# Optimization experiments

Measured on AMD Instinct MI355X. Metric: run time of the kernel, lower is better.

Reference implementation:

```python
import jax, jax.numpy as jnp
import numpy as np

B, H, N, DH = 4096, 4, 1024, 256  # batch, heads, codes per head, per-head dim
DECAY, EPS, COMMIT = 0.99, 1e-5, 0.25


def setup_inputs() -> dict:
    key = jax.random.key(0)
    k1, k2, k3, k4 = jax.random.split(key, 4)
    return {
        "inputs": jax.random.normal(k1, (B, 1, H * DH), dtype=jnp.float32),
        "emb_w": jax.random.normal(k2, (H, N, DH), dtype=jnp.float32),
        "ema_w": jax.random.normal(k3, (H, N, DH), dtype=jnp.float32),
        "cluster_size": jnp.zeros((H, N), dtype=jnp.float32),
        "trans_w": jax.random.normal(k4, (H, N, N), dtype=jnp.float32) * 0.03,
    }


def reference(inputs, emb_w, ema_w, cluster_size, trans_w):
    sg = jax.lax.stop_gradient
    x = inputs[:, 0, :].reshape(B, H, DH)  # split heads
    quant, codes = [], []
    prev_probs = None
    for h in range(H):
        xi = x[:, h]                       # [B, DH]
        w = emb_w[h]                       # [N, DH]
        # squared euclidean distances [B, N]
        d = (jnp.sum(xi * xi, axis=1, keepdims=True)
             + jnp.sum(w * w, axis=1)
             - 2.0 * xi @ w.T)
        logits = -sg(d)
        if prev_probs is not None:  # transition prior from previous head (detached)
            logits = logits + sg(prev_probs @ trans_w[h].T)
        probs = jax.nn.softmax(logits, axis=-1)
        prev_probs = probs
        # EMA codebook update (training mode)
        cs = cluster_size[h] * DECAY + (1.0 - DECAY) * jnp.sum(probs, axis=0)
        n = jnp.sum(cs)
        cs = (cs + EPS) / (n + N * EPS) * n
        dw = probs.T @ xi                  # [N, DH]
        ew = ema_w[h] * DECAY + (1.0 - DECAY) * dw
        new_w = ew / cs[:, None]           # updated codebook used for quantization
        codes.append(jnp.argmax(probs, axis=-1))
        quant.append(probs @ sg(new_w))    # soft-EM quantization, detached codebook
    quantized = jnp.stack(quant, axis=1).reshape(inputs.shape)  # [B,1,H*DH]
    q_loss = jnp.mean((quantized - sg(inputs)) ** 2, axis=(-1, -2))
    e_loss = jnp.mean((sg(quantized) - inputs) ** 2, axis=(-1, -2))
    loss = COMMIT * e_loss + q_loss        # [B]
    quantized = inputs + sg(quantized - inputs)  # straight-through
    vq_codes = jnp.stack(codes, axis=1)    # [B, H]
    return loss, quantized, vq_codes
```

## Files before the change

### kernel.cpp

```cpp
#include <hip/hip_runtime.h>
#include <hip/hip_bf16.h>
#include <math.h>

#define BB 4096
#define HH 4
#define NN 1024
#define DHD 256
#define XLD 1024
#define DECAY 0.99f
#define OMD 0.01f
#define EPSV 1e-5f

typedef __attribute__((ext_vector_type(8))) short bf16x8;
typedef __attribute__((ext_vector_type(4))) float f32x4;
typedef unsigned short u16;

#define MFMA(a, b, c) __builtin_amdgcn_mfma_f32_16x16x32_bf16((a), (b), (c), 0, 0, 0)


static __device__ __forceinline__ u16 f2bf(float x) {
    union { __hip_bfloat16 b; u16 u; } c; c.b = __float2bfloat16(x); return c.u;
}
static __device__ __forceinline__ float bf2f(u16 u) {
    union { __hip_bfloat16 b; u16 u; } c; c.u = u; return __bfloat162float(c.b);
}
static __device__ __forceinline__ void split3(float x, u16& h, u16& m, u16& l) {
    h = f2bf(x);
    float r = x - bf2f(h);
    m = f2bf(r);
    float r2 = r - bf2f(m);
    l = f2bf(r2);
}

__global__ __launch_bounds__(256) void k_prep_x(const float* __restrict__ in,
        u16* __restrict__ xph, u16* __restrict__ xpm, u16* __restrict__ xpl,
        u16* __restrict__ xtph, u16* __restrict__ xtpl) {
    __shared__ float T[64][68];
    const int t = threadIdx.x, lane = t & 63, wid = t >> 6;
    const int q = lane >> 4, mr = lane & 15;
    const int c0 = blockIdx.x * 64, i0 = blockIdx.y * 64;
    const int h = c0 >> 8, kl0 = c0 & 255;
#pragma unroll
    for (int rep = 0; rep < 4; rep++) {
        int id = t + 256 * rep;
        int row = id >> 4, c4 = (id & 15) * 4;
        float4 v = *(const float4*)(in + (size_t)(i0 + row) * XLD + c0 + c4);
        *(float4*)&T[row][c4] = v;
    }
    __syncthreads();
    for (int f = wid; f < 8; f += 4) {
        int a = f >> 1, b = f & 1;
        bf16x8 vh, vm, vl;
#pragma unroll
        for (int e = 0; e < 8; e++) {
            float x2 = 2.f * T[16 * a + mr][b * 32 + q * 8 + e];
            u16 hh, mm, ll; split3(x2, hh, mm, ll);
            vh[e] = (short)hh; vm[e] = (short)mm; vl[e] = (short)ll;
        }
        size_t o = (size_t)h * BB * DHD +
                   ((size_t)((i0 >> 4) + a) * 8 + ((kl0 >> 5) + b)) * 512 + lane * 8;
        *(bf16x8*)(xph + o) = vh;
        *(bf16x8*)(xpm + o) = vm;
        *(bf16x8*)(xpl + o) = vl;
    }
    for (int f = wid; f < 8; f += 4) {
        int a = f >> 1, b = f & 1;
        bf16x8 vh, vl;
#pragma unroll
        for (int e = 0; e < 8; e++) {
            float x = T[b * 32 + q * 8 + e][16 * a + mr];
            u16 hh = f2bf(x);
            u16 ll = f2bf(x - bf2f(hh));
            vh[e] = (short)hh; vl[e] = (short)ll;
        }
        size_t o = (size_t)h * DHD * BB +
                   ((size_t)((kl0 >> 4) + a) * 128 + ((i0 >> 5) + b)) * 512 + lane * 8;
        *(bf16x8*)(xtph + o) = vh;
        *(bf16x8*)(xtpl + o) = vl;
    }
}

__global__ __launch_bounds__(256) void k_prep_w(const float* __restrict__ w,
        u16* __restrict__ wph, u16* __restrict__ wpm, u16* __restrict__ wpl) {
    const int t = threadIdx.x, lane = t & 63, wid = t >> 6;
    const int q = lane >> 4, mr = lane & 15;
    int fid = blockIdx.x * 4 + wid;
    int kt = fid & 7, jt = (fid >> 3) & 63, h = fid >> 9;
    const float* src = w + (size_t)(h * NN + jt * 16 + mr) * DHD + kt * 32 + q * 8;
    bf16x8 vh, vm, vl;
#pragma unroll
    for (int e = 0; e < 8; e++) {
        u16 hh, mm, ll; split3(src[e], hh, mm, ll);
        vh[e] = (short)hh; vm[e] = (short)mm; vl[e] = (short)ll;
    }
    size_t o = (size_t)h * NN * DHD + ((size_t)jt * 8 + kt) * 512 + lane * 8;
    *(bf16x8*)(wph + o) = vh;
    *(bf16x8*)(wpm + o) = vm;
    *(bf16x8*)(wpl + o) = vl;
}

__global__ __launch_bounds__(256) void k_prep_t(const float* __restrict__ w,
        u16* __restrict__ tph, u16* __restrict__ tpl) {
    const int t = threadIdx.x, lane = t & 63, wid = t >> 6;
    const int q = lane >> 4, mr = lane & 15;
    int fid = blockIdx.x * 4 + wid;
    int kt = fid & 31, jt = (fid >> 5) & 63, h = fid >> 11;
    const float* src = w + (size_t)(h * NN + jt * 16 + mr) * NN + kt * 32 + q * 8;
    bf16x8 vh, vl;
#pragma unroll
    for (int e = 0; e < 8; e++) {
        u16 hh = f2bf(src[e]);
        u16 ll = f2bf(src[e] - bf2f(hh));
        vh[e] = (short)hh; vl[e] = (short)ll;
    }
    size_t o = (size_t)h * NN * NN + ((size_t)jt * 32 + kt) * 512 + lane * 8;
    *(bf16x8*)(tph + o) = vh;
    *(bf16x8*)(tpl + o) = vl;
}

__global__ __launch_bounds__(256) void k_wsq(const float* __restrict__ emb,
                                             float* __restrict__ wsq) {
    int wave = threadIdx.x >> 6;
    int lane = threadIdx.x & 63;
    int row  = blockIdx.x * 4 + wave;
    const float* w = emb + (size_t)row * DHD;
    float4 v = *(const float4*)(w + lane * 4);
    float s = v.x * v.x + v.y * v.y + v.z * v.z + v.w * v.w;
    for (int off = 32; off; off >>= 1) s += __shfl_down(s, off);
    if (lane == 0) wsq[row] = s;
}

template <int HASPREV>
__global__ __launch_bounds__(256) void k_logits_frag(
        const u16* __restrict__ Xph, const u16* __restrict__ Xpm, const u16* __restrict__ Xpl,
        const u16* __restrict__ Wph, const u16* __restrict__ Wpm, const u16* __restrict__ Wpl,
        const float* __restrict__ wsq,
        const u16* __restrict__ Pph, const u16* __restrict__ Ppl,
        const u16* __restrict__ Tph, const u16* __restrict__ Tpl,
        float* __restrict__ L) {
    const int t = threadIdx.x;
    const int lane = t & 63, wid = t >> 6;
    const int wmi = wid >> 1, wn = wid & 1;
    const int q = lane >> 4, mr = lane & 15;
    const int j0 = blockIdx.x * 64, i0 = blockIdx.y * 64;
    const int it0 = (i0 >> 4) + wmi * 2;
    const int jt0 = (j0 >> 4) + wn * 2;
    const int lo = lane * 8;

    f32x4 zero = {0.f, 0.f, 0.f, 0.f};
    f32x4 s[2][2], acc2[2][2];
#pragma unroll
    for (int mt = 0; mt < 2; mt++)
#pragma unroll
        for (int nt = 0; nt < 2; nt++) { s[mt][nt] = zero; acc2[mt][nt] = zero; }

    {
        const u16 *ahp[2], *amp[2], *alp[2], *bhp[2], *bmp[2], *blp[2];
#pragma unroll
        for (int mt = 0; mt < 2; mt++) {
            size_t b = (size_t)(it0 + mt) * 8 * 512 + lo;
            ahp[mt] = Xph + b; amp[mt] = Xpm + b; alp[mt] = Xpl + b;
        }
#pragma unroll
        for (int nt = 0; nt < 2; nt++) {
            size_t b = (size_t)(jt0 + nt) * 8 * 512 + lo;
            bhp[nt] = Wph + b; bmp[nt] = Wpm + b; blp[nt] = Wpl + b;
        }
#pragma unroll 2
        for (int kt = 0; kt < 8; kt++) {
            bf16x8 ah[2], am[2], al[2], bh[2], bm[2], bl[2];
#pragma unroll
            for (int mt = 0; mt < 2; mt++) {
                ah[mt] = *(const bf16x8*)(ahp[mt] + kt * 512);
                am[mt] = *(const bf16x8*)(amp[mt] + kt * 512);
                al[mt] = *(const bf16x8*)(alp[mt] + kt * 512);
            }
#pragma unroll
            for (int nt = 0; nt < 2; nt++) {
                bh[nt] = *(const bf16x8*)(bhp[nt] + kt * 512);
                bm[nt] = *(const bf16x8*)(bmp[nt] + kt * 512);
                bl[nt] = *(const bf16x8*)(blp[nt] + kt * 512);
            }
#pragma unroll
            for (int mt = 0; mt < 2; mt++)
#pragma unroll
                for (int nt = 0; nt < 2; nt++) {
                    f32x4 fresh = MFMA(ah[mt], bh[nt], zero);
                    s[mt][nt] += fresh;
                    acc2[mt][nt] = MFMA(ah[mt], bm[nt], acc2[mt][nt]);
                    acc2[mt][nt] = MFMA(am[mt], bh[nt], acc2[mt][nt]);
                    acc2[mt][nt] = MFMA(ah[mt], bl[nt], acc2[mt][nt]);
                    acc2[mt][nt] = MFMA(am[mt], bm[nt], acc2[mt][nt]);
                    acc2[mt][nt] = MFMA(al[mt], bh[nt], acc2[mt][nt]);
                }
        }
    }

    if (HASPREV) {
        const u16 *ahp[2], *alp[2], *bhp[2], *blp[2];
#pragma unroll
        for (int mt = 0; mt < 2; mt++) {
            size_t b = (size_t)(it0 + mt) * 32 * 512 + lo;
            ahp[mt] = Pph + b; alp[mt] = Ppl + b;
        }
#pragma unroll
        for (int nt = 0; nt < 2; nt++) {
            size_t b = (size_t)(jt0 + nt) * 32 * 512 + lo;
            bhp[nt] = Tph + b; blp[nt] = Tpl + b;
        }
#pragma unroll 2
        for (int kt = 0; kt < 32; kt++) {
            bf16x8 ah[2], al[2], bh[2], bl[2];
#pragma unroll
            for (int mt = 0; mt < 2; mt++) {
                ah[mt] = *(const bf16x8*)(ahp[mt] + kt * 512);
                al[mt] = *(const bf16x8*)(alp[mt] + kt * 512);
            }
#pragma unroll
            for (int nt = 0; nt < 2; nt++) {
                bh[nt] = *(const bf16x8*)(bhp[nt] + kt * 512);
                bl[nt] = *(const bf16x8*)(blp[nt] + kt * 512);
            }
#pragma unroll
            for (int mt = 0; mt < 2; mt++)
#pragma unroll
                for (int nt = 0; nt < 2; nt++) {
                    acc2[mt][nt] = MFMA(ah[mt], bh[nt], acc2[mt][nt]);
                    acc2[mt][nt] = MFMA(ah[mt], bl[nt], acc2[mt][nt]);
                    acc2[mt][nt] = MFMA(al[mt], bh[nt], acc2[mt][nt]);
                }
        }
    }

    float wq[2];
#pragma unroll
    for (int nt = 0; nt < 2; nt++) wq[nt] = wsq[j0 + wn * 32 + nt * 16 + mr];
#pragma unroll
    for (int mt = 0; mt < 2; mt++)
#pragma unroll
        for (int nt = 0; nt < 2; nt++)
#pragma unroll
            for (int r = 0; r < 4; r++) {
                int gi = i0 + wmi * 32 + mt * 16 + q * 4 + r;
                int gj = j0 + wn * 32 + nt * 16 + mr;
                L[(size_t)gi * NN + gj] = (s[mt][nt][r] + acc2[mt][nt][r]) - wq[nt];
            }
}

__global__ __launch_bounds__(256) void k_softmax(const float* __restrict__ L,
                                                 u16* __restrict__ Ph,
                                                 u16* __restrict__ Pl,
                                                 float* __restrict__ codes,
                                                 int h) {
    __shared__ float smax[256];
    __shared__ int   sidx[256];
    const int i = blockIdx.x;
    const int t = threadIdx.x;
    const float* row = L + (size_t)i * NN;

    float v[4];
    float m = -INFINITY;
    int   mi = 0;
#pragma unroll
    for (int q4 = 0; q4 < 4; q4++) {
        int j = q4 * 256 + t;
        v[q4] = row[j];
        if (v[q4] > m) { m = v[q4]; mi = j; }
    }
    smax[t] = m; sidx[t] = mi;
    __syncthreads();
    for (int s = 128; s; s >>= 1) {
        if (t < s) {
            float o = smax[t + s]; int oi = sidx[t + s];
            if (o > smax[t] || (o == smax[t] && oi < sidx[t])) { smax[t] = o; sidx[t] = oi; }
        }
        __syncthreads();
    }
    m = smax[0];
    int code = sidx[0];
    __syncthreads();

    float s = 0.f;
#pragma unroll
    for (int q4 = 0; q4 < 4; q4++) { v[q4] = expf(v[q4] - m); s += v[q4]; }
    smax[t] = s;
    __syncthreads();
    for (int ss = 128; ss; ss >>= 1) {
        if (t < ss) smax[t] += smax[t + ss];
        __syncthreads();
    }
    float inv = 1.0f / smax[0];
#pragma unroll
    for (int q4 = 0; q4 < 4; q4++) {
        float pv = v[q4] * inv;
        u16 hb = f2bf(pv);
        Ph[(size_t)i * NN + q4 * 256 + t] = hb;
        Pl[(size_t)i * NN + q4 * 256 + t] = f2bf(pv - bf2f(hb));
    }
    if (t == 0) codes[(size_t)i * HH + h] = (float)code;
}

__global__ __launch_bounds__(256) void k_packP(const u16* __restrict__ Ph,
        const u16* __restrict__ Pl, u16* __restrict__ Pph, u16* __restrict__ Ppl) {
    const int t = threadIdx.x, lane = t & 63, wid = t >> 6;
    const int q = lane >> 4, mr = lane & 15;
    int fid = blockIdx.x * 4 + wid;
    int kt = fid & 31, it = fid >> 5;
    size_t si = (size_t)(it * 16 + mr) * NN + kt * 32 + q * 8;
    bf16x8 vh = *(const bf16x8*)(Ph + si);
    bf16x8 vl = *(const bf16x8*)(Pl + si);
    size_t o = ((size_t)it * 32 + kt) * 512 + lane * 8;
    *(bf16x8*)(Pph + o) = vh;
    *(bf16x8*)(Ppl + o) = vl;
}

__global__ __launch_bounds__(256) void k_packPT(const u16* __restrict__ Ph,
        const u16* __restrict__ Pl, u16* __restrict__ PTph, u16* __restrict__ PTpl) {
    __shared__ u16 U[64][72];
    const int t = threadIdx.x, lane = t & 63, wid = t >> 6;
    const int q = lane >> 4, mr = lane & 15;
    const int j0 = blockIdx.x * 64, i0 = blockIdx.y * 64;
    for (int pass = 0; pass < 2; pass++) {
        const u16* src = pass ? Pl : Ph;
        u16* dst = pass ? PTpl : PTph;
        if (pass) __syncthreads();
#pragma unroll
        for (int rep = 0; rep < 2; rep++) {
            int id = t + 256 * rep;
            int row = id >> 3, c8 = (id & 7) * 8;
            *(bf16x8*)&U[row][c8] = *(const bf16x8*)(src + (size_t)(i0 + row) * NN + j0 + c8);
        }
        __syncthreads();
        for (int f = wid; f < 8; f += 4) {
            int a = f >> 1, b = f & 1;
            bf16x8 v;
#pragma unroll
            for (int e = 0; e < 8; e++) v[e] = (short)U[b * 32 + q * 8 + e][16 * a + mr];
            size_t o = ((size_t)((j0 >> 4) + a) * 128 + ((i0 >> 5) + b)) * 512 + lane * 8;
            *(bf16x8*)(dst + o) = v;
        }
    }
}

__global__ __launch_bounds__(256) void k_colsum(const u16* __restrict__ Ph,
                                                const u16* __restrict__ Pl,
                                                float* __restrict__ colsum) {
    int j  = blockIdx.x * 256 + threadIdx.x;
    int i0 = blockIdx.y * 256;
    float s = 0.f;
    for (int i = i0; i < i0 + 256; i++)
        s += bf2f(Ph[(size_t)i * NN + j]) + bf2f(Pl[(size_t)i * NN + j]);
    atomicAdd(&colsum[j], s);
}

__global__ __launch_bounds__(1024) void k_cs(const float* __restrict__ cluster_size,
                                             const float* __restrict__ colsum,
                                             float* __restrict__ csn, int h) {
    __shared__ float red[1024];
    int j = threadIdx.x;
    float cs = cluster_size[h * NN + j] * DECAY + OMD * colsum[j];
    red[j] = cs;
    __syncthreads();
    for (int s = 512; s; s >>= 1) {
        if (j < s) red[j] += red[j + s];
        __syncthreads();
    }
    float n = red[0];
    csn[j] = (cs + EPSV) / (n + NN * EPSV) * n;
}

__global__ __launch_bounds__(256) void k_dw_frag(
        const u16* __restrict__ PTph, const u16* __restrict__ PTpl,
        const u16* __restrict__ XTph, const u16* __restrict__ XTpl,
        float* __restrict__ partial) {
    const int t = threadIdx.x;
    const int lane = t & 63, wid = t >> 6;
    const int wmi = wid >> 1, wn = wid & 1;
    const int q = lane >> 4, mr = lane & 15;
    const int kd0 = blockIdx.x * 64, j0 = blockIdx.y * 64;
    const int z = blockIdx.z;
    const int jt0 = (j0 >> 4) + wmi * 2;
    const int kdt0 = (kd0 >> 4) + wn * 2;
    const int lo = lane * 8;

    f32x4 zero = {0.f, 0.f, 0.f, 0.f};
    f32x4 acc[2][2];
#pragma unroll
    for (int mt = 0; mt < 2; mt++)
#pragma unroll
        for (int nt = 0; nt < 2; nt++) acc[mt][nt] = zero;

    const u16 *ahp[2], *alp[2], *bhp[2], *blp[2];
#pragma unroll
    for (int mt = 0; mt < 2; mt++) {
        size_t b = ((size_t)(jt0 + mt) * 128 + z * 8) * 512 + lo;
        ahp[mt] = PTph + b; alp[mt] = PTpl + b;
    }
#pragma unroll
    for (int nt = 0; nt < 2; nt++) {
        size_t b = ((size_t)(kdt0 + nt) * 128 + z * 8) * 512 + lo;
        bhp[nt] = XTph + b; blp[nt] = XTpl + b;
    }
#pragma unroll 2
    for (int kt = 0; kt < 8; kt++) {
        bf16x8 ah[2], al[2], bh[2], bl[2];
#pragma unroll
        for (int mt = 0; mt < 2; mt++) {
            ah[mt] = *(const bf16x8*)(ahp[mt] + kt * 512);
            al[mt] = *(const bf16x8*)(alp[mt] + kt * 512);
        }
#pragma unroll
        for (int nt = 0; nt < 2; nt++) {
            bh[nt] = *(const bf16x8*)(bhp[nt] + kt * 512);
            bl[nt] = *(const bf16x8*)(blp[nt] + kt * 512);
        }
#pragma unroll
        for (int mt = 0; mt < 2; mt++)
#pragma unroll
            for (int nt = 0; nt < 2; nt++) {
                acc[mt][nt] = MFMA(ah[mt], bh[nt], acc[mt][nt]);
                acc[mt][nt] = MFMA(ah[mt], bl[nt], acc[mt][nt]);
                acc[mt][nt] = MFMA(al[mt], bh[nt], acc[mt][nt]);
            }
    }
#pragma unroll
    for (int mt = 0; mt < 2; mt++)
#pragma unroll
        for (int nt = 0; nt < 2; nt++)
#pragma unroll
            for (int r = 0; r < 4; r++) {
                int gj = j0 + wmi * 32 + mt * 16 + q * 4 + r;
                int gk = kd0 + wn * 32 + nt * 16 + mr;
                atomicAdd(&partial[(size_t)gj * DHD + gk], acc[mt][nt][r]);
            }
}

__global__ __launch_bounds__(256) void k_neww_ep(const float* __restrict__ partial,
        const float* __restrict__ ema, const float* __restrict__ csn,
        u16* __restrict__ NWph, u16* __restrict__ NWpl) {
    __shared__ float T[64][68];
    const int t = threadIdx.x, lane = t & 63, wid = t >> 6;
    const int q = lane >> 4, mr = lane & 15;
    const int j0 = blockIdx.x * 64, kd0 = blockIdx.y * 64;
#pragma unroll
    for (int rep = 0; rep < 4; rep++) {
        int id = t + 256 * rep;
        int jr = id >> 4, c4 = (id & 15) * 4;
        float4 pp = *(const float4*)(partial + (size_t)(j0 + jr) * DHD + kd0 + c4);
        float4 ee = *(const float4*)(ema + (size_t)(j0 + jr) * DHD + kd0 + c4);
        float ic = 1.0f / csn[j0 + jr];
        float4 v;
        v.x = (ee.x * DECAY + OMD * pp.x) * ic;
        v.y = (ee.y * DECAY + OMD * pp.y) * ic;
        v.z = (ee.z * DECAY + OMD * pp.z) * ic;
        v.w = (ee.w * DECAY + OMD * pp.w) * ic;
        *(float4*)&T[jr][c4] = v;
    }
    __syncthreads();
    for (int f = wid; f < 8; f += 4) {
        int a = f >> 1, b = f & 1;
        bf16x8 vh, vl;
#pragma unroll
        for (int e = 0; e < 8; e++) {
            float x = T[b * 32 + q * 8 + e][16 * a + mr];
            u16 hh = f2bf(x);
            u16 ll = f2bf(x - bf2f(hh));
            vh[e] = (short)hh; vl[e] = (short)ll;
        }
        size_t o = ((size_t)((kd0 >> 4) + a) * 32 + ((j0 >> 5) + b)) * 512 + lane * 8;
        *(bf16x8*)(NWph + o) = vh;
        *(bf16x8*)(NWpl + o) = vl;
    }
}

__global__ __launch_bounds__(256) void k_quant_frag(
        const u16* __restrict__ Pph, const u16* __restrict__ Ppl,
        const u16* __restrict__ NWph, const u16* __restrict__ NWpl,
        float* __restrict__ outq, int h) {
    const int t = threadIdx.x;
    const int lane = t & 63, wid = t >> 6;
    const int wmi = wid >> 1, wn = wid & 1;
    const int q = lane >> 4, mr = lane & 15;
    const int kd0 = blockIdx.x * 64, i0 = blockIdx.y * 64;
    const int z = blockIdx.z;
    const int it0 = (i0 >> 4) + wmi * 2;
    const int kdt0 = (kd0 >> 4) + wn * 2;
    const int lo = lane * 8;

    f32x4 zero = {0.f, 0.f, 0.f, 0.f};
    f32x4 acc[2][2];
#pragma unroll
    for (int mt = 0; mt < 2; mt++)
#pragma unroll
        for (int nt = 0; nt < 2; nt++) acc[mt][nt] = zero;

    const u16 *ahp[2], *alp[2], *bhp[2], *blp[2];
#pragma unroll
    for (int mt = 0; mt < 2; mt++) {
        size_t b = ((size_t)(it0 + mt) * 32 + z * 8) * 512 + lo;
        ahp[mt] = Pph + b; alp[mt] = Ppl + b;
    }
#pragma unroll
    for (int nt = 0; nt < 2; nt++) {
        size_t b = ((size_t)(kdt0 + nt) * 32 + z * 8) * 512 + lo;
        bhp[nt] = NWph + b; blp[nt] = NWpl + b;
    }
#pragma unroll 2
    for (int kt = 0; kt < 8; kt++) {
        bf16x8 ah[2], al[2], bh[2], bl[2];
#pragma unroll
        for (int mt = 0; mt < 2; mt++) {
            ah[mt] = *(const bf16x8*)(ahp[mt] + kt * 512);
            al[mt] = *(const bf16x8*)(alp[mt] + kt * 512);
        }
#pragma unroll
        for (int nt = 0; nt < 2; nt++) {
            bh[nt] = *(const bf16x8*)(bhp[nt] + kt * 512);
            bl[nt] = *(const bf16x8*)(blp[nt] + kt * 512);
        }
#pragma unroll
        for (int mt = 0; mt < 2; mt++)
#pragma unroll
            for (int nt = 0; nt < 2; nt++) {
                acc[mt][nt] = MFMA(ah[mt], bh[nt], acc[mt][nt]);
                acc[mt][nt] = MFMA(ah[mt], bl[nt], acc[mt][nt]);
                acc[mt][nt] = MFMA(al[mt], bh[nt], acc[mt][nt]);
            }
    }
#pragma unroll
    for (int mt = 0; mt < 2; mt++)
#pragma unroll
        for (int nt = 0; nt < 2; nt++)
#pragma unroll
            for (int r = 0; r < 4; r++) {
                int gi = i0 + wmi * 32 + mt * 16 + q * 4 + r;
                int gk = kd0 + wn * 32 + nt * 16 + mr;
                atomicAdd(&outq[(size_t)gi * XLD + h * DHD + gk], acc[mt][nt][r]);
            }
}

__global__ __launch_bounds__(256) void k_loss(const float* __restrict__ x,
                                              const float* __restrict__ qv,
                                              float* __restrict__ loss) {
    __shared__ float red[256];
    const int i = blockIdx.x, t = threadIdx.x;
    const float* xr = x + (size_t)i * XLD;
    const float* qr = qv + (size_t)i * XLD;
    float s = 0.f;
#pragma unroll
    for (int q4 = 0; q4 < 4; q4++) {
        int k = q4 * 256 + t;
        float d = qr[k] - xr[k];
        s += d * d;
    }
    red[t] = s;
    __syncthreads();
    for (int ss = 128; ss; ss >>= 1) {
        if (t < ss) red[t] += red[t + ss];
        __syncthreads();
    }
    if (t == 0) loss[i] = 1.25f * red[0] * (1.0f / 1024.0f);
}

extern "C" void kernel_launch(void* const* d_in, const int* in_sizes, int n_in,
                              void* d_out, int out_size, void* d_ws, size_t ws_size,
                              hipStream_t stream) {
    const float* inputs = (const float*)d_in[0];
    const float* emb    = (const float*)d_in[1];
    const float* ema    = (const float*)d_in[2];
    const float* csz    = (const float*)d_in[3];
    const float* trans  = (const float*)d_in[4];

    float* out   = (float*)d_out;
    float* loss  = out;
    float* quant = out + BB;
    float* codes = out + BB + (size_t)BB * XLD;

    char* p = (char*)d_ws;
    float* L = (float*)p; p += (size_t)BB * NN * 4;
    u16* PTph = (u16*)L;
    u16* PTpl = PTph + (size_t)BB * NN;
    u16* Ph   = (u16*)p; p += (size_t)BB * NN * 2;
    u16* Pl   = (u16*)p; p += (size_t)BB * NN * 2;
    u16* Pph  = (u16*)p; p += (size_t)BB * NN * 2;
    u16* Ppl  = (u16*)p; p += (size_t)BB * NN * 2;
    u16* Xph  = (u16*)p; p += (size_t)BB * XLD * 2;
    u16* Xpm  = (u16*)p; p += (size_t)BB * XLD * 2;
    u16* Xpl  = (u16*)p; p += (size_t)BB * XLD * 2;
    u16* XTph = (u16*)p; p += (size_t)XLD * BB * 2;
    u16* XTpl = (u16*)p; p += (size_t)XLD * BB * 2;
    u16* Wph  = (u16*)p; p += (size_t)HH * NN * DHD * 2;
    u16* Wpm  = (u16*)p; p += (size_t)HH * NN * DHD * 2;
    u16* Wpl  = (u16*)p; p += (size_t)HH * NN * DHD * 2;
    u16* Tph  = (u16*)p; p += (size_t)HH * NN * NN * 2;
    u16* Tpl  = (u16*)p; p += (size_t)HH * NN * NN * 2;
    u16* NWph = (u16*)p; p += (size_t)DHD * NN * 2;
    u16* NWpl = (u16*)p; p += (size_t)DHD * NN * 2;
    float* wsq    = (float*)p; p += (size_t)HH * NN * 4;
    float* colsum = (float*)p; p += NN * 4;
    float* csn    = (float*)p; p += NN * 4;
    float* partial = (float*)p; p += (size_t)NN * DHD * 4;

    k_prep_x<<<dim3(XLD / 64, BB / 64), 256, 0, stream>>>(inputs, Xph, Xpm, Xpl, XTph, XTpl);
    k_prep_w<<<HH * 64 * 8 / 4, 256, 0, stream>>>(emb, Wph, Wpm, Wpl);
    k_prep_t<<<HH * 64 * 32 / 4, 256, 0, stream>>>(trans, Tph, Tpl);
    k_wsq<<<HH * NN / 4, 256, 0, stream>>>(emb, wsq);
    hipMemsetAsync(quant, 0, (size_t)BB * XLD * 4, stream);

    for (int h = 0; h < HH; h++) {
        const u16* Xhh = Xph + (size_t)h * BB * DHD;
        const u16* Xmh = Xpm + (size_t)h * BB * DHD;
        const u16* Xlh = Xpl + (size_t)h * BB * DHD;
        const u16* Whh = Wph + (size_t)h * NN * DHD;
        const u16* Wmh = Wpm + (size_t)h * NN * DHD;
        const u16* Wlh = Wpl + (size_t)h * NN * DHD;
        if (h == 0)
            k_logits_frag<0><<<dim3(NN / 64, BB / 64), 256, 0, stream>>>(
                Xhh, Xmh, Xlh, Whh, Wmh, Wlh, wsq + h * NN,
                nullptr, nullptr, nullptr, nullptr, L);
        else
            k_logits_frag<1><<<dim3(NN / 64, BB / 64), 256, 0, stream>>>(
                Xhh, Xmh, Xlh, Whh, Wmh, Wlh, wsq + h * NN,
                Pph, Ppl, Tph + (size_t)h * NN * NN, Tpl + (size_t)h * NN * NN, L);

        k_softmax<<<BB, 256, 0, stream>>>(L, Ph, Pl, codes, h);
        k_packP<<<BB / 16 * NN / 32 / 4, 256, 0, stream>>>(Ph, Pl, Pph, Ppl);
        k_packPT<<<dim3(NN / 64, BB / 64), 256, 0, stream>>>(Ph, Pl, PTph, PTpl);

        hipMemsetAsync(colsum, 0, NN * sizeof(float), stream);
        k_colsum<<<dim3(NN / 256, 16), 256, 0, stream>>>(Ph, Pl, colsum);
        k_cs<<<1, NN, 0, stream>>>(csz, colsum, csn, h);

        hipMemsetAsync(partial, 0, (size_t)NN * DHD * sizeof(float), stream);
        k_dw_frag<<<dim3(DHD / 64, NN / 64, 16), 256, 0, stream>>>(
            PTph, PTpl, XTph + (size_t)h * DHD * BB, XTpl + (size_t)h * DHD * BB, partial);
        k_neww_ep<<<dim3(NN / 64, DHD / 64), 256, 0, stream>>>(
            partial, ema + (size_t)h * NN * DHD, csn, NWph, NWpl);

        k_quant_frag<<<dim3(DHD / 64, BB / 64, 4), 256, 0, stream>>>(
            Pph, Ppl, NWph, NWpl, quant, h);
    }

    k_loss<<<BB, 256, 0, stream>>>(inputs, quant, loss);
}
```

Baseline: 669.6 us.

## Split logits into two kernels, fuse P packing with colsum, replace atomics with split-K scratch

The logits kernel is split into a distance pass and a separate transition-prior pass. The prior pass uses split-K over two z-slices and atomically accumulates into L, which raises parallelism for the 1024-deep prior GEMM. The packP, packPT and colsum kernels are merged into one shared-memory tile kernel that reads P once. The dw and quant GEMMs now write per-slice partials to scratch and reduce them in epilogue kernels instead of using float atomics and memsets. The trade-off is extra scratch traffic and kernel launches in exchange for fewer global reads and less atomic contention.

```diff
diff --git a/kernel.cpp b/kernel.cpp
--- a/kernel.cpp
+++ b/kernel.cpp
@@ -130,11 +130,82 @@
     if (lane == 0) wsq[row] = s;
 }
 
-template <int HASPREV>
-__global__ __launch_bounds__(256) void k_logits_frag(
+__global__ __launch_bounds__(256) void k_logits_p1(
         const u16* __restrict__ Xph, const u16* __restrict__ Xpm, const u16* __restrict__ Xpl,
         const u16* __restrict__ Wph, const u16* __restrict__ Wpm, const u16* __restrict__ Wpl,
-        const float* __restrict__ wsq,
+        const float* __restrict__ wsq, float* __restrict__ L) {
+    const int t = threadIdx.x;
+    const int lane = t & 63, wid = t >> 6;
+    const int wmi = wid >> 1, wn = wid & 1;
+    const int q = lane >> 4, mr = lane & 15;
+    const int j0 = blockIdx.x * 64, i0 = blockIdx.y * 64;
+    const int it0 = (i0 >> 4) + wmi * 2;
+    const int jt0 = (j0 >> 4) + wn * 2;
+    const int lo = lane * 8;
+
+    f32x4 zero = {0.f, 0.f, 0.f, 0.f};
+    f32x4 s[2][2], acc2[2][2];
+#pragma unroll
+    for (int mt = 0; mt < 2; mt++)
+#pragma unroll
+        for (int nt = 0; nt < 2; nt++) { s[mt][nt] = zero; acc2[mt][nt] = zero; }
+
+    const u16 *ahp[2], *amp[2], *alp[2], *bhp[2], *bmp[2], *blp[2];
+#pragma unroll
+    for (int mt = 0; mt < 2; mt++) {
+        size_t b = (size_t)(it0 + mt) * 8 * 512 + lo;
+        ahp[mt] = Xph + b; amp[mt] = Xpm + b; alp[mt] = Xpl + b;
+    }
+#pragma unroll
+    for (int nt = 0; nt < 2; nt++) {
+        size_t b = (size_t)(jt0 + nt) * 8 * 512 + lo;
+        bhp[nt] = Wph + b; bmp[nt] = Wpm + b; blp[nt] = Wpl + b;
+    }
+#pragma unroll 2
+    for (int kt = 0; kt < 8; kt++) {
+        bf16x8 ah[2], am[2], al[2], bh[2], bm[2], bl[2];
+#pragma unroll
+        for (int mt = 0; mt < 2; mt++) {
+            ah[mt] = *(const bf16x8*)(ahp[mt] + kt * 512);
+            am[mt] = *(const bf16x8*)(amp[mt] + kt * 512);
+            al[mt] = *(const bf16x8*)(alp[mt] + kt * 512);
+        }
+#pragma unroll
+        for (int nt = 0; nt < 2; nt++) {
+            bh[nt] = *(const bf16x8*)(bhp[nt] + kt * 512);
+            bm[nt] = *(const bf16x8*)(bmp[nt] + kt * 512);
+            bl[nt] = *(const bf16x8*)(blp[nt] + kt * 512);
+        }
+#pragma unroll
+        for (int mt = 0; mt < 2; mt++)
+#pragma unroll
+            for (int nt = 0; nt < 2; nt++) {
+                f32x4 fresh = MFMA(ah[mt], bh[nt], zero);
+                s[mt][nt] += fresh;
+                acc2[mt][nt] = MFMA(ah[mt], bm[nt], acc2[mt][nt]);
+                acc2[mt][nt] = MFMA(am[mt], bh[nt], acc2[mt][nt]);
+                acc2[mt][nt] = MFMA(ah[mt], bl[nt], acc2[mt][nt]);
+                acc2[mt][nt] = MFMA(am[mt], bm[nt], acc2[mt][nt]);
+                acc2[mt][nt] = MFMA(al[mt], bh[nt], acc2[mt][nt]);
+            }
+    }
+
+    float wq[2];
+#pragma unroll
+    for (int nt = 0; nt < 2; nt++) wq[nt] = wsq[j0 + wn * 32 + nt * 16 + mr];
+#pragma unroll
+    for (int mt = 0; mt < 2; mt++)
+#pragma unroll
+        for (int nt = 0; nt < 2; nt++)
+#pragma unroll
+            for (int r = 0; r < 4; r++) {
+                int gi = i0 + wmi * 32 + mt * 16 + q * 4 + r;
+                int gj = j0 + wn * 32 + nt * 16 + mr;
+                L[(size_t)gi * NN + gj] = (s[mt][nt][r] + acc2[mt][nt][r]) - wq[nt];
+            }
+}
+
+__global__ __launch_bounds__(256) void k_logits_p2(
         const u16* __restrict__ Pph, const u16* __restrict__ Ppl,
         const u16* __restrict__ Tph, const u16* __restrict__ Tpl,
         float* __restrict__ L) {
@@ -143,98 +214,51 @@
     const int wmi = wid >> 1, wn = wid & 1;
     const int q = lane >> 4, mr = lane & 15;
     const int j0 = blockIdx.x * 64, i0 = blockIdx.y * 64;
+    const int kz = blockIdx.z;
     const int it0 = (i0 >> 4) + wmi * 2;
     const int jt0 = (j0 >> 4) + wn * 2;
     const int lo = lane * 8;
 
     f32x4 zero = {0.f, 0.f, 0.f, 0.f};
-    f32x4 s[2][2], acc2[2][2];
-#pragma unroll
-    for (int mt = 0; mt < 2; mt++)
-#pragma unroll
-        for (int nt = 0; nt < 2; nt++) { s[mt][nt] = zero; acc2[mt][nt] = zero; }
-
-    {
-        const u16 *ahp[2], *amp[2], *alp[2], *bhp[2], *bmp[2], *blp[2];
+    f32x4 acc2[2][2];
+#pragma unroll
+    for (int mt = 0; mt < 2; mt++)
+#pragma unroll
+        for (int nt = 0; nt < 2; nt++) acc2[mt][nt] = zero;
+
+    const u16 *ahp[2], *alp[2], *bhp[2], *blp[2];
+#pragma unroll
+    for (int mt = 0; mt < 2; mt++) {
+        size_t b = ((size_t)(it0 + mt) * 32 + kz * 16) * 512 + lo;
+        ahp[mt] = Pph + b; alp[mt] = Ppl + b;
+    }
+#pragma unroll
+    for (int nt = 0; nt < 2; nt++) {
+        size_t b = ((size_t)(jt0 + nt) * 32 + kz * 16) * 512 + lo;
+        bhp[nt] = Tph + b; blp[nt] = Tpl + b;
+    }
+#pragma unroll 4
+    for (int kt = 0; kt < 16; kt++) {
+        bf16x8 ah[2], al[2], bh[2], bl[2];
 #pragma unroll
         for (int mt = 0; mt < 2; mt++) {
-            size_t b = (size_t)(it0 + mt) * 8 * 512 + lo;
-            ahp[mt] = Xph + b; amp[mt] = Xpm + b; alp[mt] = Xpl + b;
+            ah[mt] = *(const bf16x8*)(ahp[mt] + kt * 512);
+            al[mt] = *(const bf16x8*)(alp[mt] + kt * 512);
         }
 #pragma unroll
         for (int nt = 0; nt < 2; nt++) {
-            size_t b = (size_t)(jt0 + nt) * 8 * 512 + lo;
-            bhp[nt] = Wph + b; bmp[nt] = Wpm + b; blp[nt] = Wpl + b;
-        }
-#pragma unroll 2
-        for (int kt = 0; kt < 8; kt++) {
-            bf16x8 ah[2], am[2], al[2], bh[2], bm[2], bl[2];
-#pragma unroll
-            for (int mt = 0; mt < 2; mt++) {
-                ah[mt] = *(const bf16x8*)(ahp[mt] + kt * 512);
-                am[mt] = *(const bf16x8*)(amp[mt] + kt * 512);
-                al[mt] = *(const bf16x8*)(alp[mt] + kt * 512);
-            }
+            bh[nt] = *(const bf16x8*)(bhp[nt] + kt * 512);
+            bl[nt] = *(const bf16x8*)(blp[nt] + kt * 512);
+        }
+#pragma unroll
+        for (int mt = 0; mt < 2; mt++)
 #pragma unroll
             for (int nt = 0; nt < 2; nt++) {
-                bh[nt] = *(const bf16x8*)(bhp[nt] + kt * 512);
-                bm[nt] = *(const bf16x8*)(bmp[nt] + kt * 512);
-                bl[nt] = *(const bf16x8*)(blp[nt] + kt * 512);
-            }
-#pragma unroll
-            for (int mt = 0; mt < 2; mt++)
-#pragma unroll
-                for (int nt = 0; nt < 2; nt++) {
-                    f32x4 fresh = MFMA(ah[mt], bh[nt], zero);
-                    s[mt][nt] += fresh;
-                    acc2[mt][nt] = MFMA(ah[mt], bm[nt], acc2[mt][nt]);
-                    acc2[mt][nt] = MFMA(am[mt], bh[nt], acc2[mt][nt]);
-                    acc2[mt][nt] = MFMA(ah[mt], bl[nt], acc2[mt][nt]);
-                    acc2[mt][nt] = MFMA(am[mt], bm[nt], acc2[mt][nt]);
-                    acc2[mt][nt] = MFMA(al[mt], bh[nt], acc2[mt][nt]);
-                }
-        }
-    }
-
-    if (HASPREV) {
-        const u16 *ahp[2], *alp[2], *bhp[2], *blp[2];
-#pragma unroll
-        for (int mt = 0; mt < 2; mt++) {
-            size_t b = (size_t)(it0 + mt) * 32 * 512 + lo;
-            ahp[mt] = Pph + b; alp[mt] = Ppl + b;
-        }
-#pragma unroll
-        for (int nt = 0; nt < 2; nt++) {
-            size_t b = (size_t)(jt0 + nt) * 32 * 512 + lo;
-            bhp[nt] = Tph + b; blp[nt] = Tpl + b;
-        }
-#pragma unroll 2
-        for (int kt = 0; kt < 32; kt++) {
-            bf16x8 ah[2], al[2], bh[2], bl[2];
-#pragma unroll
-            for (int mt = 0; mt < 2; mt++) {
-                ah[mt] = *(const bf16x8*)(ahp[mt] + kt * 512);
-                al[mt] = *(const bf16x8*)(alp[mt] + kt * 512);
-            }
-#pragma unroll
-            for (int nt = 0; nt < 2; nt++) {
-                bh[nt] = *(const bf16x8*)(bhp[nt] + kt * 512);
-                bl[nt] = *(const bf16x8*)(blp[nt] + kt * 512);
-            }
-#pragma unroll
-            for (int mt = 0; mt < 2; mt++)
-#pragma unroll
-                for (int nt = 0; nt < 2; nt++) {
-                    acc2[mt][nt] = MFMA(ah[mt], bh[nt], acc2[mt][nt]);
-                    acc2[mt][nt] = MFMA(ah[mt], bl[nt], acc2[mt][nt]);
-                    acc2[mt][nt] = MFMA(al[mt], bh[nt], acc2[mt][nt]);
-                }
-        }
-    }
-
-    float wq[2];
-#pragma unroll
-    for (int nt = 0; nt < 2; nt++) wq[nt] = wsq[j0 + wn * 32 + nt * 16 + mr];
+                acc2[mt][nt] = MFMA(ah[mt], bh[nt], acc2[mt][nt]);
+                acc2[mt][nt] = MFMA(ah[mt], bl[nt], acc2[mt][nt]);
+                acc2[mt][nt] = MFMA(al[mt], bh[nt], acc2[mt][nt]);
+            }
+    }
 #pragma unroll
     for (int mt = 0; mt < 2; mt++)
 #pragma unroll
@@ -243,7 +267,7 @@
             for (int r = 0; r < 4; r++) {
                 int gi = i0 + wmi * 32 + mt * 16 + q * 4 + r;
                 int gj = j0 + wn * 32 + nt * 16 + mr;
-                L[(size_t)gi * NN + gj] = (s[mt][nt][r] + acc2[mt][nt][r]) - wq[nt];
+                atomicAdd(&L[(size_t)gi * NN + gj], acc2[mt][nt][r]);
             }
 }
 
@@ -300,57 +324,59 @@
     if (t == 0) codes[(size_t)i * HH + h] = (float)code;
 }
 
-__global__ __launch_bounds__(256) void k_packP(const u16* __restrict__ Ph,
-        const u16* __restrict__ Pl, u16* __restrict__ Pph, u16* __restrict__ Ppl) {
+__global__ __launch_bounds__(256) void k_packcs(const u16* __restrict__ Ph,
+        const u16* __restrict__ Pl,
+        u16* __restrict__ Pph, u16* __restrict__ Ppl,
+        u16* __restrict__ PTph, u16* __restrict__ PTpl,
+        float* __restrict__ colsum) {
+    __shared__ u16 Uh[64][72], Ul[64][72];
+    __shared__ float red[4][64];
     const int t = threadIdx.x, lane = t & 63, wid = t >> 6;
     const int q = lane >> 4, mr = lane & 15;
-    int fid = blockIdx.x * 4 + wid;
-    int kt = fid & 31, it = fid >> 5;
-    size_t si = (size_t)(it * 16 + mr) * NN + kt * 32 + q * 8;
-    bf16x8 vh = *(const bf16x8*)(Ph + si);
-    bf16x8 vl = *(const bf16x8*)(Pl + si);
-    size_t o = ((size_t)it * 32 + kt) * 512 + lane * 8;
-    *(bf16x8*)(Pph + o) = vh;
-    *(bf16x8*)(Ppl + o) = vl;
-}
-
-__global__ __launch_bounds__(256) void k_packPT(const u16* __restrict__ Ph,
-        const u16* __restrict__ Pl, u16* __restrict__ PTph, u16* __restrict__ PTpl) {
-    __shared__ u16 U[64][72];
-    const int t = threadIdx.x, lane = t & 63, wid = t >> 6;
-    const int q = lane >> 4, mr = lane & 15;
     const int j0 = blockIdx.x * 64, i0 = blockIdx.y * 64;
-    for (int pass = 0; pass < 2; pass++) {
-        const u16* src = pass ? Pl : Ph;
-        u16* dst = pass ? PTpl : PTph;
-        if (pass) __syncthreads();
-#pragma unroll
-        for (int rep = 0; rep < 2; rep++) {
-            int id = t + 256 * rep;
-            int row = id >> 3, c8 = (id & 7) * 8;
-            *(bf16x8*)&U[row][c8] = *(const bf16x8*)(src + (size_t)(i0 + row) * NN + j0 + c8);
-        }
-        __syncthreads();
-        for (int f = wid; f < 8; f += 4) {
-            int a = f >> 1, b = f & 1;
-            bf16x8 v;
-#pragma unroll
-            for (int e = 0; e < 8; e++) v[e] = (short)U[b * 32 + q * 8 + e][16 * a + mr];
-            size_t o = ((size_t)((j0 >> 4) + a) * 128 + ((i0 >> 5) + b)) * 512 + lane * 8;
-            *(bf16x8*)(dst + o) = v;
-        }
-    }
-}
-
-__global__ __launch_bounds__(256) void k_colsum(const u16* __restrict__ Ph,
-                                                const u16* __restrict__ Pl,
-                                                float* __restrict__ colsum) {
-    int j  = blockIdx.x * 256 + threadIdx.x;
-    int i0 = blockIdx.y * 256;
+#pragma unroll
+    for (int rep = 0; rep < 2; rep++) {
+        int id = t + 256 * rep;
+        int row = id >> 3, c8 = (id & 7) * 8;
+        size_t si = (size_t)(i0 + row) * NN + j0 + c8;
+        *(bf16x8*)&Uh[row][c8] = *(const bf16x8*)(Ph + si);
+        *(bf16x8*)&Ul[row][c8] = *(const bf16x8*)(Pl + si);
+    }
+    __syncthreads();
+    for (int f = wid; f < 8; f += 4) {
+        int a = f >> 1, b = f & 1;
+        bf16x8 vh, vl;
+#pragma unroll
+        for (int e = 0; e < 8; e++) {
+            vh[e] = Uh[a * 16 + mr][b * 32 + q * 8 + e];
+            vl[e] = Ul[a * 16 + mr][b * 32 + q * 8 + e];
+        }
+        size_t o = ((size_t)((i0 >> 4) + a) * 32 + ((j0 >> 5) + b)) * 512 + lane * 8;
+        *(bf16x8*)(Pph + o) = vh;
+        *(bf16x8*)(Ppl + o) = vl;
+    }
+    for (int f = wid; f < 8; f += 4) {
+        int a = f >> 1, b = f & 1;
+        bf16x8 vh, vl;
+#pragma unroll
+        for (int e = 0; e < 8; e++) {
+            vh[e] = Uh[b * 32 + q * 8 + e][a * 16 + mr];
+            vl[e] = Ul[b * 32 + q * 8 + e][a * 16 + mr];
+        }
+        size_t o = ((size_t)((j0 >> 4) + a) * 128 + ((i0 >> 5) + b)) * 512 + lane * 8;
+        *(bf16x8*)(PTph + o) = vh;
+        *(bf16x8*)(PTpl + o) = vl;
+    }
+    int c = t & 63, quarter = t >> 6;
     float s = 0.f;
-    for (int i = i0; i < i0 + 256; i++)
-        s += bf2f(Ph[(size_t)i * NN + j]) + bf2f(Pl[(size_t)i * NN + j]);
-    atomicAdd(&colsum[j], s);
+    for (int r = quarter * 16; r < quarter * 16 + 16; r++)
+        s += bf2f((u16)Uh[r][c]) + bf2f((u16)Ul[r][c]);
+    red[quarter][c] = s;
+    __syncthreads();
+    if (t < 64) {
+        float tot = red[0][t] + red[1][t] + red[2][t] + red[3][t];
+        atomicAdd(&colsum[j0 + t], tot);
+    }
 }
 
 __global__ __launch_bounds__(1024) void k_cs(const float* __restrict__ cluster_size,
@@ -372,7 +398,7 @@
 __global__ __launch_bounds__(256) void k_dw_frag(
         const u16* __restrict__ PTph, const u16* __restrict__ PTpl,
         const u16* __restrict__ XTph, const u16* __restrict__ XTpl,
-        float* __restrict__ partial) {
+        float* __restrict__ partial16) {
     const int t = threadIdx.x;
     const int lane = t & 63, wid = t >> 6;
     const int wmi = wid >> 1, wn = wid & 1;
@@ -423,6 +449,7 @@
                 acc[mt][nt] = MFMA(al[mt], bh[nt], acc[mt][nt]);
             }
     }
+    float* dst = partial16 + (size_t)z * NN * DHD;
 #pragma unroll
     for (int mt = 0; mt < 2; mt++)
 #pragma unroll
@@ -431,11 +458,11 @@
             for (int r = 0; r < 4; r++) {
                 int gj = j0 + wmi * 32 + mt * 16 + q * 4 + r;
                 int gk = kd0 + wn * 32 + nt * 16 + mr;
-                atomicAdd(&partial[(size_t)gj * DHD + gk], acc[mt][nt][r]);
-            }
-}
-
-__global__ __launch_bounds__(256) void k_neww_ep(const float* __restrict__ partial,
+                dst[(size_t)gj * DHD + gk] = acc[mt][nt][r];
+            }
+}
+
+__global__ __launch_bounds__(256) void k_neww_ep(const float* __restrict__ partial16,
         const float* __restrict__ ema, const float* __restrict__ csn,
         u16* __restrict__ NWph, u16* __restrict__ NWpl) {
     __shared__ float T[64][68];
@@ -446,14 +473,19 @@
     for (int rep = 0; rep < 4; rep++) {
         int id = t + 256 * rep;
         int jr = id >> 4, c4 = (id & 15) * 4;
-        float4 pp = *(const float4*)(partial + (size_t)(j0 + jr) * DHD + kd0 + c4);
-        float4 ee = *(const float4*)(ema + (size_t)(j0 + jr) * DHD + kd0 + c4);
+        size_t off = (size_t)(j0 + jr) * DHD + kd0 + c4;
+        float4 acc = {0.f, 0.f, 0.f, 0.f};
+        for (int z = 0; z < 16; z++) {
+            float4 pp = *(const float4*)(partial16 + (size_t)z * NN * DHD + off);
+            acc.x += pp.x; acc.y += pp.y; acc.z += pp.z; acc.w += pp.w;
+        }
+        float4 ee = *(const float4*)(ema + off);
         float ic = 1.0f / csn[j0 + jr];
         float4 v;
-        v.x = (ee.x * DECAY + OMD * pp.x) * ic;
-        v.y = (ee.y * DECAY + OMD * pp.y) * ic;
-        v.z = (ee.z * DECAY + OMD * pp.z) * ic;
-        v.w = (ee.w * DECAY + OMD * pp.w) * ic;
+        v.x = (ee.x * DECAY + OMD * acc.x) * ic;
+        v.y = (ee.y * DECAY + OMD * acc.y) * ic;
+        v.z = (ee.z * DECAY + OMD * acc.z) * ic;
+        v.w = (ee.w * DECAY + OMD * acc.w) * ic;
         *(float4*)&T[jr][c4] = v;
     }
     __syncthreads();
@@ -476,7 +508,7 @@
 __global__ __launch_bounds__(256) void k_quant_frag(
         const u16* __restrict__ Pph, const u16* __restrict__ Ppl,
         const u16* __restrict__ NWph, const u16* __restrict__ NWpl,
-        float* __restrict__ outq, int h) {
+        float* __restrict__ qacc4) {
     const int t = threadIdx.x;
     const int lane = t & 63, wid = t >> 6;
     const int wmi = wid >> 1, wn = wid & 1;
@@ -527,6 +559,7 @@
                 acc[mt][nt] = MFMA(al[mt], bh[nt], acc[mt][nt]);
             }
     }
+    float* dst = qacc4 + (size_t)z * BB * DHD;
 #pragma unroll
     for (int mt = 0; mt < 2; mt++)
 #pragma unroll
@@ -535,8 +568,21 @@
             for (int r = 0; r < 4; r++) {
                 int gi = i0 + wmi * 32 + mt * 16 + q * 4 + r;
                 int gk = kd0 + wn * 32 + nt * 16 + mr;
-                atomicAdd(&outq[(size_t)gi * XLD + h * DHD + gk], acc[mt][nt][r]);
-            }
+                dst[(size_t)gi * DHD + gk] = acc[mt][nt][r];
+            }
+}
+
+__global__ __launch_bounds__(256) void k_quant_ep(const float* __restrict__ qacc4,
+        float* __restrict__ outq, int h) {
+    int idx4 = (blockIdx.x * 256 + threadIdx.x) * 4;
+    int i = idx4 >> 8, kd = idx4 & 255;
+    float4 s = {0.f, 0.f, 0.f, 0.f};
+#pragma unroll
+    for (int z = 0; z < 4; z++) {
+        float4 v = *(const float4*)(qacc4 + (size_t)z * BB * DHD + idx4);
+        s.x += v.x; s.y += v.y; s.z += v.z; s.w += v.w;
+    }
+    *(float4*)(outq + (size_t)i * XLD + h * DHD + kd) = s;
 }
 
 __global__ __launch_bounds__(256) void k_loss(const float* __restrict__ x,
@@ -599,13 +645,12 @@
     float* wsq    = (float*)p; p += (size_t)HH * NN * 4;
     float* colsum = (float*)p; p += NN * 4;
     float* csn    = (float*)p; p += NN * 4;
-    float* partial = (float*)p; p += (size_t)NN * DHD * 4;
+    float* scratch16 = (float*)p; p += (size_t)16 * NN * DHD * 4;
 
     k_prep_x<<<dim3(XLD / 64, BB / 64), 256, 0, stream>>>(inputs, Xph, Xpm, Xpl, XTph, XTpl);
     k_prep_w<<<HH * 64 * 8 / 4, 256, 0, stream>>>(emb, Wph, Wpm, Wpl);
     k_prep_t<<<HH * 64 * 32 / 4, 256, 0, stream>>>(trans, Tph, Tpl);
     k_wsq<<<HH * NN / 4, 256, 0, stream>>>(emb, wsq);
-    hipMemsetAsync(quant, 0, (size_t)BB * XLD * 4, stream);
 
     for (int h = 0; h < HH; h++) {
         const u16* Xhh = Xph + (size_t)h * BB * DHD;
@@ -614,31 +659,29 @@
         const u16* Whh = Wph + (size_t)h * NN * DHD;
         const u16* Wmh = Wpm + (size_t)h * NN * DHD;
         const u16* Wlh = Wpl + (size_t)h * NN * DHD;
-        if (h == 0)
-            k_logits_frag<0><<<dim3(NN / 64, BB / 64), 256, 0, stream>>>(
-                Xhh, Xmh, Xlh, Whh, Wmh, Wlh, wsq + h * NN,
-                nullptr, nullptr, nullptr, nullptr, L);
-        else
-            k_logits_frag<1><<<dim3(NN / 64, BB / 64), 256, 0, stream>>>(
-                Xhh, Xmh, Xlh, Whh, Wmh, Wlh, wsq + h * NN,
+
+        k_logits_p1<<<dim3(NN / 64, BB / 64), 256, 0, stream>>>(
+            Xhh, Xmh, Xlh, Whh, Wmh, Wlh, wsq + h * NN, L);
+        if (h > 0)
+            k_logits_p2<<<dim3(NN / 64, BB / 64, 2), 256, 0, stream>>>(
                 Pph, Ppl, Tph + (size_t)h * NN * NN, Tpl + (size_t)h * NN * NN, L);
 
         k_softmax<<<BB, 256, 0, stream>>>(L, Ph, Pl, codes, h);
-        k_packP<<<BB / 16 * NN / 32 / 4, 256, 0, stream>>>(Ph, Pl, Pph, Ppl);
-        k_packPT<<<dim3(NN / 64, BB / 64), 256, 0, stream>>>(Ph, Pl, PTph, PTpl);
 
         hipMemsetAsync(colsum, 0, NN * sizeof(float), stream);
-        k_colsum<<<dim3(NN / 256, 16), 256, 0, stream>>>(Ph, Pl, colsum);
+        k_packcs<<<dim3(NN / 64, BB / 64), 256, 0, stream>>>(
+            Ph, Pl, Pph, Ppl, PTph, PTpl, colsum);
         k_cs<<<1, NN, 0, stream>>>(csz, colsum, csn, h);
 
-        hipMemsetAsync(partial, 0, (size_t)NN * DHD * sizeof(float), stream);
         k_dw_frag<<<dim3(DHD / 64, NN / 64, 16), 256, 0, stream>>>(
-            PTph, PTpl, XTph + (size_t)h * DHD * BB, XTpl + (size_t)h * DHD * BB, partial);
+            PTph, PTpl, XTph + (size_t)h * DHD * BB, XTpl + (size_t)h * DHD * BB,
+            scratch16);
         k_neww_ep<<<dim3(NN / 64, DHD / 64), 256, 0, stream>>>(
-            partial, ema + (size_t)h * NN * DHD, csn, NWph, NWpl);
+            scratch16, ema + (size_t)h * NN * DHD, csn, NWph, NWpl);
 
         k_quant_frag<<<dim3(DHD / 64, BB / 64, 4), 256, 0, stream>>>(
-            Pph, Ppl, NWph, NWpl, quant, h);
+            Pph, Ppl, NWph, NWpl, scratch16);
+        k_quant_ep<<<BB * DHD / 1024, 256, 0, stream>>>(scratch16, quant, h);
     }
 
     k_loss<<<BB, 256, 0, stream>>>(inputs, quant, loss);
```

Result: faster. 598.7 us (-10.6%).
